# Kernel optimization log

Measured on AMD Instinct MI355X. Metric: run time of the kernel, lower is better.

The kernel has to match this reference:

```python
import jax, jax.numpy as jnp
import numpy as np

D_IN = 784
D_Z = 100
N_SAMP = 10
LOG_2PI = float(np.log(2.0 * np.pi))


def setup_inputs() -> dict:
    key = jax.random.key(0)
    ks = jax.random.split(key, 8)
    B = 16384
    x = jax.random.uniform(ks[0], (B, D_IN), dtype=jnp.float32)
    s = 0.05  # small init scale so softplus/sigmoid stay in a sane range
    W0 = jax.random.normal(ks[1], (D_Z, D_IN), dtype=jnp.float32) * s
    b0 = jax.random.normal(ks[2], (D_Z,), dtype=jnp.float32) * s
    W1 = jax.random.normal(ks[3], (D_Z, D_IN), dtype=jnp.float32) * s
    b1 = jax.random.normal(ks[4], (D_Z,), dtype=jnp.float32) * s
    W2 = jax.random.normal(ks[5], (D_IN, D_Z), dtype=jnp.float32) * s
    b2 = jax.random.normal(ks[6], (D_IN,), dtype=jnp.float32) * s
    eps = jax.random.normal(ks[7], (N_SAMP, D_Z), dtype=jnp.float32)  # pz.sample([10])
    return {"x": x, "W0": W0, "b0": b0, "W1": W1, "b1": b1, "W2": W2, "b2": b2, "eps": eps}


def reference(x, W0, b0, W1, b1, W2, b2, eps):
    # encoder: per-dim mean over the batch of softplus(Linear(x))
    mean = jnp.mean(jax.nn.softplus(x @ W0.T + b0), axis=0)        # [D_Z]
    cov = jnp.mean(jax.nn.softplus(x @ W1.T + b1), axis=0)         # [D_Z] (diag variances)
    # z = mean + covariance * eps, eps ~ N(0, I)
    z = mean + cov * eps                                           # [N_SAMP, D_Z]
    y = z @ W2.T + b2                                              # [N_SAMP, D_IN]
    p = jax.nn.sigmoid((2.0 * x[:, None, :] - 1.0) * y[None, :, :])  # [B, N_SAMP, D_IN]
    pv_z = jnp.prod(p, axis=-1) + 0.001                            # [B, N_SAMP]
    E_px_v = jnp.mean(jnp.log(pv_z))
    # diagonal-Gaussian log probs (equivalent to the MVN with eye*cov)
    log_pz = -0.5 * jnp.sum(z * z, axis=-1) - 0.5 * D_Z * LOG_2PI
    log_q = (-0.5 * jnp.sum((z - mean) ** 2 / cov, axis=-1)
             - 0.5 * jnp.sum(jnp.log(cov)) - 0.5 * D_Z * LOG_2PI)
    Dkl = jnp.mean(log_pz - log_q)
    return -(E_px_v + Dkl)
```

## Files before the change

kernel.cpp:

```cpp
#include <hip/hip_runtime.h>
#include <hip/hip_bf16.h>
#include <math.h>

#define NROWS 16384
#define DIN   784
#define DZ    100
#define NS    10
#define NCT   16
#define KTILES 25
#define BND_THR 45.0f
#define KTPAD 520

typedef unsigned short ushort_t;
typedef short bf16x8 __attribute__((ext_vector_type(8)));
typedef float f32x4  __attribute__((ext_vector_type(4)));

#define WS_Y2 208
#define WB_OFF_BYTES (64u * 1024u)

__device__ __forceinline__ float softplus_fast(float v) {
    float t = v * 1.44269504088896f;
    return (fmaxf(t, 0.f)
            + __builtin_amdgcn_logf(1.f + __builtin_amdgcn_exp2f(-fabsf(t))))
           * 0.69314718055995f;
}
__device__ __forceinline__ unsigned pack2(float lo, float hi) {
    float2 f2; f2.x = lo; f2.y = hi;
    __hip_bfloat162 h2 = __float22bfloat162_rn(f2);
    return *reinterpret_cast<unsigned*>(&h2);
}

__global__ __launch_bounds__(256) void wb_kernel(
    const float* __restrict__ W0, const float* __restrict__ W1,
    ushort_t* __restrict__ Wb, float* __restrict__ ws)
{
    if (blockIdx.x == 0) ws[threadIdx.x] = 0.f;
    int t = blockIdx.x * 256 + threadIdx.x;
    if (t >= KTILES * NCT * 64) return;
    int kt = t >> 10;
    int r  = t & 1023;
    int ct = r >> 6, l = r & 63;
    int col = ct * 16 + (l & 15);
    int k0  = kt * 32 + (l >> 4) * 8;
    uint4 o = make_uint4(0u, 0u, 0u, 0u);
    if (col < 200 && k0 < DIN) {
        const float* src = (col < 100 ? W0 + (size_t)col * DIN
                                      : W1 + (size_t)(col - 100) * DIN) + k0;
        float4 a = *(const float4*)src;
        float4 b = *(const float4*)(src + 4);
        o.x = pack2(a.x, a.y); o.y = pack2(a.z, a.w);
        o.z = pack2(b.x, b.y); o.w = pack2(b.z, b.w);
    }
    *(uint4*)(Wb + (size_t)t * 8) = o;
}

__global__ __launch_bounds__(1024) void colmean_h(
    const float* __restrict__ x, const ushort_t* __restrict__ Wb,
    const float* __restrict__ b0, const float* __restrict__ b1,
    float* __restrict__ ws)
{
    __shared__ ushort_t xls[4 * KTILES * KTPAD];
    const int tid = threadIdx.x;
    const int lane = tid & 63, w = tid >> 6;
    const int row0 = blockIdx.x * 64;

    for (int slot = tid; slot < 6400; slot += 1024) {
        int r  = slot / 100;
        int sl = slot - r * 100;
        int kt = sl >> 2, kc = sl & 3;
        int k0 = kt * 32 + kc * 8;
        uint4 o = make_uint4(0u, 0u, 0u, 0u);
        if (k0 + 8 <= DIN) {
            const float* src = x + (size_t)(row0 + r) * DIN + k0;
            float4 a = *(const float4*)src, b = *(const float4*)(src + 4);
            o.x = pack2(a.x, a.y); o.y = pack2(a.z, a.w);
            o.z = pack2(b.x, b.y); o.w = pack2(b.z, b.w);
        }
        int l = (kc << 4) | (r & 15);
        *(uint4*)&xls[((size_t)(r >> 4) * KTILES + kt) * KTPAD + l * 8] = o;
    }
    __syncthreads();

    const ushort_t* ap  = xls + lane * 8;
    const ushort_t* wbp = Wb + (size_t)w * 512 + lane * 8;

    f32x4 acc0 = (f32x4){0.f,0.f,0.f,0.f}, acc1 = acc0, acc2 = acc0, acc3 = acc0;

    bf16x8 Aa[4], Ab[4];
    uint4  Ba, Bb;

    auto ld = [&](int kt, bf16x8 (&A)[4], uint4& B) {
#pragma unroll
        for (int rt = 0; rt < 4; ++rt)
            A[rt] = *(const bf16x8*)(ap + (size_t)rt * KTILES * KTPAD + (size_t)kt * KTPAD);
        B = *(const uint4*)(wbp + (size_t)kt * 8192);
    };
    auto cp = [&](const bf16x8 (&A)[4], const uint4& B) {
        bf16x8 bf = *(const bf16x8*)&B;
        acc0 = __builtin_amdgcn_mfma_f32_16x16x32_bf16(A[0], bf, acc0, 0, 0, 0);
        acc1 = __builtin_amdgcn_mfma_f32_16x16x32_bf16(A[1], bf, acc1, 0, 0, 0);
        acc2 = __builtin_amdgcn_mfma_f32_16x16x32_bf16(A[2], bf, acc2, 0, 0, 0);
        acc3 = __builtin_amdgcn_mfma_f32_16x16x32_bf16(A[3], bf, acc3, 0, 0, 0);
    };

    ld(0, Aa, Ba);
    for (int i = 0; i < 12; ++i) {
        ld(2 * i + 1, Ab, Bb);
        cp(Aa, Ba);
        ld(2 * i + 2, Aa, Ba);
        cp(Ab, Bb);
    }
    cp(Aa, Ba);

    const int j = w * 16 + (lane & 15);
    const float bias = (j < 100) ? b0[j] : ((j < 200) ? b1[j - 100] : 0.f);
    float v = 0.f;
#pragma unroll
    for (int r = 0; r < 4; ++r)
        v += softplus_fast(acc0[r] + bias) + softplus_fast(acc1[r] + bias)
           + softplus_fast(acc2[r] + bias) + softplus_fast(acc3[r] + bias);
    v += __shfl_xor(v, 16);
    v += __shfl_xor(v, 32);
    if ((lane >> 4) == 0 && j < 200) atomicAdd(&ws[j], v);
}

__global__ __launch_bounds__(256) void y2z_kernel(
    const float* __restrict__ W2, const float* __restrict__ b2,
    const float* __restrict__ eps, float* __restrict__ ws)
{
    int wid  = (int)((blockIdx.x * 256 + threadIdx.x) >> 6);
    int lane = threadIdx.x & 63;
    if (wid >= NS * DIN) return;
    int s = wid / DIN, i = wid % DIN;
    const float inv = 1.f / (float)NROWS;
    const float* wr = W2 + (size_t)i * DZ;
    const float* er = eps + (size_t)s * DZ;
    float p = 0.f;
    for (int d = lane; d < DZ; d += 64) {
        float zd = inv * (ws[d] + ws[100 + d] * er[d]);
        p += zd * wr[d];
    }
#pragma unroll
    for (int off = 32; off > 0; off >>= 1) p += __shfl_xor(p, off);
    if (lane == 0) ws[WS_Y2 + wid] = (p + b2[i]) * 1.4426950408889634f;
}

__global__ __launch_bounds__(256, 4) void pv_final_kernel(
    const float* __restrict__ x, float* __restrict__ ws,
    const float* __restrict__ eps, float* __restrict__ out, int nblocks)
{
    __shared__ ushort_t yf[KTILES * 512];
    __shared__ ushort_t ya[KTILES * 512];
    __shared__ float bsum;
    __shared__ int lastflag;
    __shared__ float dred[256];
    const int tid = threadIdx.x;
    const int lane = tid & 63, w = tid >> 6;

    for (int idx = tid; idx < KTILES * 64; idx += 256) {
        int kt = idx >> 6, l = idx & 63;
        int ss = l & 15, k0 = kt * 32 + (l >> 4) * 8;
        uint4 o = make_uint4(0u, 0u, 0u, 0u), oa = o;
        if (ss < NS && k0 < DIN) {
            const float* src = ws + WS_Y2 + ss * DIN + k0;
            float4 a = *(const float4*)src, b = *(const float4*)(src + 4);
            o.x = pack2(a.x, a.y); o.y = pack2(a.z, a.w);
            o.z = pack2(b.x, b.y); o.w = pack2(b.z, b.w);
            oa.x = o.x & 0x7FFF7FFFu; oa.y = o.y & 0x7FFF7FFFu;
            oa.z = o.z & 0x7FFF7FFFu; oa.w = o.w & 0x7FFF7FFFu;
        }
        *(uint4*)(yf + (size_t)idx * 8) = o;
        *(uint4*)(ya + (size_t)idx * 8) = oa;
    }
    if (tid == 0) { bsum = 0.f; lastflag = 0; }
    __syncthreads();

    const int tile = blockIdx.x * 4 + w;
    const int row  = tile * 16 + (lane & 15);
    const int kc   = lane >> 4;
    const int s    = lane & 15;
    const float* xp = x + (size_t)row * DIN;
    const float L001 = -6.90775527898f;

    f32x4 acc0 = (f32x4){0.f, 0.f, 0.f, 0.f};
    f32x4 acc1 = (f32x4){0.f, 0.f, 0.f, 0.f};
    float4 a0A, a1A, a0B, a1B;

    auto loadA = [&](int kt, float4& a0, float4& a1) {
        int k0 = kt * 32 + kc * 8;
        if (k0 + 8 > DIN) k0 = 768;
        a0 = *(const float4*)(xp + k0);
        a1 = *(const float4*)(xp + k0 + 4);
    };
    auto comp = [&](int kt, const float4& a0, const float4& a1) {
        bf16x8 nf; unsigned* p = (unsigned*)&nf;
        p[0] = pack2(1.f - 2.f * a0.x, 1.f - 2.f * a0.y);
        p[1] = pack2(1.f - 2.f * a0.z, 1.f - 2.f * a0.w);
        p[2] = pack2(1.f - 2.f * a1.x, 1.f - 2.f * a1.y);
        p[3] = pack2(1.f - 2.f * a1.z, 1.f - 2.f * a1.w);
        bf16x8 na; unsigned* q = (unsigned*)&na;
        q[0] = p[0] & 0x7FFF7FFFu; q[1] = p[1] & 0x7FFF7FFFu;
        q[2] = p[2] & 0x7FFF7FFFu; q[3] = p[3] & 0x7FFF7FFFu;
        bf16x8 fy = *(const bf16x8*)(yf + (size_t)kt * 512 + lane * 8);
        bf16x8 fa = *(const bf16x8*)(ya + (size_t)kt * 512 + lane * 8);
        acc0 = __builtin_amdgcn_mfma_f32_16x16x32_bf16(nf, fy, acc0, 0, 0, 0);
        acc1 = __builtin_amdgcn_mfma_f32_16x16x32_bf16(na, fa, acc1, 0, 0, 0);
    };
    loadA(0, a0A, a1A);
    for (int i = 0; i < 12; ++i) {
        loadA(2 * i + 1, a0B, a1B);
        comp(2 * i, a0A, a1A);
        loadA(2 * i + 2, a0A, a1A);
        comp(2 * i + 1, a0B, a1B);
    }
    comp(24, a0A, a1A);

    float bnd[4];
#pragma unroll
    for (int r = 0; r < 4; ++r) bnd[r] = 0.5f * (acc0[r] + acc1[r]);
    float wsum;
    bool lslow = (s < NS) &&
        (fminf(fminf(bnd[0], bnd[1]), fminf(bnd[2], bnd[3])) < BND_THR);
    unsigned long long m = __ballot(lslow);
    if (m == 0ull) {
        wsum = 160.f * L001;
    } else {
        int nslow = 0;
        float slowsum = 0.f;
#pragma unroll
        for (int r = 0; r < 4; ++r) {
            unsigned long long mr = __ballot((s < NS) && (bnd[r] < BND_THR));
            nslow += (int)__popcll(mr);
            while (mr) {
                int src = (int)__ffsll(mr) - 1; mr &= (mr - 1);
                int ss = src & 15;
                int rrow = tile * 16 + (src >> 4) * 4 + r;
                const float* xq = x + (size_t)rrow * DIN;
                const float* yq = ws + WS_Y2 + ss * DIN;
                float a = 0.f;
                for (int i = lane; i < DIN; i += 64)
                    a -= __builtin_amdgcn_logf(
                        1.f + __builtin_amdgcn_exp2f((1.f - 2.f * xq[i]) * yq[i]));
#pragma unroll
                for (int off = 32; off > 0; off >>= 1) a += __shfl_xor(a, off);
                slowsum += __logf(__builtin_amdgcn_exp2f(a) + 0.001f);
            }
        }
        wsum = (float)(160 - nslow) * L001 + slowsum;
    }
    if (lane == 0) atomicAdd(&bsum, wsum);
    __syncthreads();

    if (tid == 0) {
        atomicAdd(&ws[200], bsum);
        __threadfence();
        unsigned old = atomicAdd((unsigned*)&ws[203], 1u);
        if (old == (unsigned)(nblocks - 1)) lastflag = 1;
    }
    __syncthreads();
    if (lastflag) {
        __threadfence();
        float contrib = 0.f;
        if (tid < DZ) {
            const float inv = 1.f / (float)NROWS;
            float mm = ws[tid] * inv;
            float cc = ws[100 + tid] * inv;
            contrib = 0.5f * __logf(cc);
#pragma unroll
            for (int ss2 = 0; ss2 < NS; ++ss2) {
                float e = eps[ss2 * DZ + tid];
                float zz = mm + cc * e;
                contrib += (0.5f * cc * e * e - 0.5f * zz * zz) * (1.f / NS);
            }
        }
        dred[tid] = contrib;
        __syncthreads();
        for (int off = 128; off > 0; off >>= 1) {
            if (tid < off) dred[tid] += dred[tid + off];
            __syncthreads();
        }
        if (tid == 0) {
            float S = atomicAdd(&ws[200], 0.f);
            float E = S * (1.f / ((float)NROWS * (float)NS));
            out[0] = -(E + dred[0]);
        }
    }
}

extern "C" void kernel_launch(void* const* d_in, const int* in_sizes, int n_in,
                              void* d_out, int out_size, void* d_ws, size_t ws_size,
                              hipStream_t stream)
{
    const float* x   = (const float*)d_in[0];
    const float* W0  = (const float*)d_in[1];
    const float* b0  = (const float*)d_in[2];
    const float* W1  = (const float*)d_in[3];
    const float* b1  = (const float*)d_in[4];
    const float* W2  = (const float*)d_in[5];
    const float* b2  = (const float*)d_in[6];
    const float* eps = (const float*)d_in[7];
    float* out = (float*)d_out;
    float* ws  = (float*)d_ws;
    ushort_t* Wb = (ushort_t*)((char*)d_ws + WB_OFF_BYTES);

    wb_kernel<<<(KTILES * NCT * 64 + 255) / 256, 256, 0, stream>>>(W0, W1, Wb, ws);
    colmean_h<<<NROWS / 64, 1024, 0, stream>>>(x, Wb, b0, b1, ws);
    y2z_kernel<<<(NS * DIN * 64) / 256, 256, 0, stream>>>(W2, b2, eps, ws);
    pv_final_kernel<<<256, 256, 0, stream>>>(x, ws, eps, out, 256);
}
```

Baseline: 50.86 us.

## Double-buffer x chunks in LDS to overlap global loads with MFMA

```diff
diff --git a/kernel.cpp b/kernel.cpp
--- a/kernel.cpp
+++ b/kernel.cpp
@@ -10,6 +10,8 @@
 #define KTILES 25
 #define BND_THR 45.0f
 #define KTPAD 520
+#define CH    5
+#define NCH   5
 
 typedef unsigned short ushort_t;
 typedef short bf16x8 __attribute__((ext_vector_type(8)));
@@ -54,63 +56,89 @@
     *(uint4*)(Wb + (size_t)t * 8) = o;
 }
 
-__global__ __launch_bounds__(1024) void colmean_h(
+__global__ __launch_bounds__(1024) void colmean_k(
     const float* __restrict__ x, const ushort_t* __restrict__ Wb,
     const float* __restrict__ b0, const float* __restrict__ b1,
     float* __restrict__ ws)
 {
-    __shared__ ushort_t xls[4 * KTILES * KTPAD];
+    __shared__ ushort_t xch[2][4 * CH * KTPAD];
     const int tid = threadIdx.x;
     const int lane = tid & 63, w = tid >> 6;
-    const int row0 = blockIdx.x * 64;
-
-    for (int slot = tid; slot < 6400; slot += 1024) {
-        int r  = slot / 100;
-        int sl = slot - r * 100;
-        int kt = sl >> 2, kc = sl & 3;
-        int k0 = kt * 32 + kc * 8;
+
+    int b = blockIdx.x;
+    int logical = (b & 7) * 32 + (b >> 3);
+    const int row0 = logical * 64;
+    const float* xr = x + (size_t)row0 * DIN;
+
+    auto stage_load = [&](int ck, int slot, uint4& s, int& doff) {
+        int r = slot / 20;
+        int rem = slot - r * 20;
+        int kt_l = rem >> 2, kc = rem & 3;
+        int k0 = (ck * CH + kt_l) * 32 + kc * 8;
         uint4 o = make_uint4(0u, 0u, 0u, 0u);
         if (k0 + 8 <= DIN) {
-            const float* src = x + (size_t)(row0 + r) * DIN + k0;
-            float4 a = *(const float4*)src, b = *(const float4*)(src + 4);
+            const float* src = xr + (size_t)r * DIN + k0;
+            float4 a = *(const float4*)src, bb = *(const float4*)(src + 4);
             o.x = pack2(a.x, a.y); o.y = pack2(a.z, a.w);
-            o.z = pack2(b.x, b.y); o.w = pack2(b.z, b.w);
-        }
+            o.z = pack2(bb.x, bb.y); o.w = pack2(bb.z, bb.w);
+        }
+        s = o;
         int l = (kc << 4) | (r & 15);
-        *(uint4*)&xls[((size_t)(r >> 4) * KTILES + kt) * KTPAD + l * 8] = o;
+        doff = ((r >> 4) * CH + kt_l) * KTPAD + l * 8;
+    };
+
+    f32x4 acc0 = (f32x4){0.f,0.f,0.f,0.f}, acc1 = acc0, acc2 = acc0, acc3 = acc0;
+    const ushort_t* wbp = Wb + (size_t)w * 512 + lane * 8;
+
+    auto compute = [&](int ck, int buf) {
+        const ushort_t* ap = xch[buf] + lane * 8;
+        uint4 Ba = *(const uint4*)(wbp + (size_t)(ck * CH) * 8192);
+#pragma unroll
+        for (int kt_l = 0; kt_l < CH; ++kt_l) {
+            uint4 Bb;
+            if (kt_l + 1 < CH)
+                Bb = *(const uint4*)(wbp + (size_t)(ck * CH + kt_l + 1) * 8192);
+            bf16x8 bf = *(const bf16x8*)&Ba;
+            bf16x8 A0 = *(const bf16x8*)(ap + (size_t)(0 * CH + kt_l) * KTPAD);
+            bf16x8 A1 = *(const bf16x8*)(ap + (size_t)(1 * CH + kt_l) * KTPAD);
+            bf16x8 A2 = *(const bf16x8*)(ap + (size_t)(2 * CH + kt_l) * KTPAD);
+            bf16x8 A3 = *(const bf16x8*)(ap + (size_t)(3 * CH + kt_l) * KTPAD);
+            acc0 = __builtin_amdgcn_mfma_f32_16x16x32_bf16(A0, bf, acc0, 0, 0, 0);
+            acc1 = __builtin_amdgcn_mfma_f32_16x16x32_bf16(A1, bf, acc1, 0, 0, 0);
+            acc2 = __builtin_amdgcn_mfma_f32_16x16x32_bf16(A2, bf, acc2, 0, 0, 0);
+            acc3 = __builtin_amdgcn_mfma_f32_16x16x32_bf16(A3, bf, acc3, 0, 0, 0);
+            Ba = Bb;
+        }
+    };
+
+    {
+        uint4 s0, s1; int d0, d1;
+        stage_load(0, tid, s0, d0);
+        bool two = (tid < 1280 - 1024);
+        if (two) stage_load(0, tid + 1024, s1, d1);
+        *(uint4*)&xch[0][d0] = s0;
+        if (two) *(uint4*)&xch[0][d1] = s1;
     }
     __syncthreads();
 
-    const ushort_t* ap  = xls + lane * 8;
-    const ushort_t* wbp = Wb + (size_t)w * 512 + lane * 8;
-
-    f32x4 acc0 = (f32x4){0.f,0.f,0.f,0.f}, acc1 = acc0, acc2 = acc0, acc3 = acc0;
-
-    bf16x8 Aa[4], Ab[4];
-    uint4  Ba, Bb;
-
-    auto ld = [&](int kt, bf16x8 (&A)[4], uint4& B) {
-#pragma unroll
-        for (int rt = 0; rt < 4; ++rt)
-            A[rt] = *(const bf16x8*)(ap + (size_t)rt * KTILES * KTPAD + (size_t)kt * KTPAD);
-        B = *(const uint4*)(wbp + (size_t)kt * 8192);
-    };
-    auto cp = [&](const bf16x8 (&A)[4], const uint4& B) {
-        bf16x8 bf = *(const bf16x8*)&B;
-        acc0 = __builtin_amdgcn_mfma_f32_16x16x32_bf16(A[0], bf, acc0, 0, 0, 0);
-        acc1 = __builtin_amdgcn_mfma_f32_16x16x32_bf16(A[1], bf, acc1, 0, 0, 0);
-        acc2 = __builtin_amdgcn_mfma_f32_16x16x32_bf16(A[2], bf, acc2, 0, 0, 0);
-        acc3 = __builtin_amdgcn_mfma_f32_16x16x32_bf16(A[3], bf, acc3, 0, 0, 0);
-    };
-
-    ld(0, Aa, Ba);
-    for (int i = 0; i < 12; ++i) {
-        ld(2 * i + 1, Ab, Bb);
-        cp(Aa, Ba);
-        ld(2 * i + 2, Aa, Ba);
-        cp(Ab, Bb);
-    }
-    cp(Aa, Ba);
+    int cur = 0;
+#pragma unroll 1
+    for (int ck = 0; ck < NCH; ++ck) {
+        uint4 s0, s1; int d0, d1;
+        const bool more = (ck + 1 < NCH);
+        const bool two = (tid < 1280 - 1024);
+        if (more) {
+            stage_load(ck + 1, tid, s0, d0);
+            if (two) stage_load(ck + 1, tid + 1024, s1, d1);
+        }
+        compute(ck, cur);
+        if (more) {
+            *(uint4*)&xch[cur ^ 1][d0] = s0;
+            if (two) *(uint4*)&xch[cur ^ 1][d1] = s1;
+        }
+        __syncthreads();
+        cur ^= 1;
+    }
 
     const int j = w * 16 + (lane & 15);
     const float bias = (j < 100) ? b0[j] : ((j < 200) ? b1[j - 100] : 0.f);
@@ -304,7 +332,7 @@
     ushort_t* Wb = (ushort_t*)((char*)d_ws + WB_OFF_BYTES);
 
     wb_kernel<<<(KTILES * NCT * 64 + 255) / 256, 256, 0, stream>>>(W0, W1, Wb, ws);
-    colmean_h<<<NROWS / 64, 1024, 0, stream>>>(x, Wb, b0, b1, ws);
+    colmean_k<<<256, 1024, 0, stream>>>(x, Wb, b0, b1, ws);
     y2z_kernel<<<(NS * DIN * 64) / 256, 256, 0, stream>>>(W2, b2, eps, ws);
     pv_final_kernel<<<256, 256, 0, stream>>>(x, ws, eps, out, 256);
 }
```

Result: slower. 53.97 us (+6.1%).

## Switch encoder GEMM to 32x32x16 MFMA tiles with repacked weights and LDS layout

Applied to the files above, without the earlier changes.

```diff
diff --git a/kernel.cpp b/kernel.cpp
--- a/kernel.cpp
+++ b/kernel.cpp
@@ -6,14 +6,16 @@
 #define DIN   784
 #define DZ    100
 #define NS    10
-#define NCT   16
 #define KTILES 25
+#define KT32  49
+#define NCT32 7
 #define BND_THR 45.0f
-#define KTPAD 520
+#define KTP2  520
 
 typedef unsigned short ushort_t;
 typedef short bf16x8 __attribute__((ext_vector_type(8)));
 typedef float f32x4  __attribute__((ext_vector_type(4)));
+typedef float f32x16 __attribute__((ext_vector_type(16)));
 
 #define WS_Y2 208
 #define WB_OFF_BYTES (64u * 1024u)
@@ -30,20 +32,20 @@
     return *reinterpret_cast<unsigned*>(&h2);
 }
 
-__global__ __launch_bounds__(256) void wb_kernel(
+__global__ __launch_bounds__(256) void wb2_kernel(
     const float* __restrict__ W0, const float* __restrict__ W1,
     ushort_t* __restrict__ Wb, float* __restrict__ ws)
 {
     if (blockIdx.x == 0) ws[threadIdx.x] = 0.f;
     int t = blockIdx.x * 256 + threadIdx.x;
-    if (t >= KTILES * NCT * 64) return;
-    int kt = t >> 10;
-    int r  = t & 1023;
-    int ct = r >> 6, l = r & 63;
-    int col = ct * 16 + (l & 15);
-    int k0  = kt * 32 + (l >> 4) * 8;
+    if (t >= KT32 * NCT32 * 64) return;
+    int kt  = t / (NCT32 * 64);
+    int rem = t - kt * (NCT32 * 64);
+    int ct = rem >> 6, l = rem & 63;
+    int col = ct * 32 + (l & 31);
+    int k0  = kt * 16 + (l >> 5) * 8;
     uint4 o = make_uint4(0u, 0u, 0u, 0u);
-    if (col < 200 && k0 < DIN) {
+    if (col < 200) {
         const float* src = (col < 100 ? W0 + (size_t)col * DIN
                                       : W1 + (size_t)(col - 100) * DIN) + k0;
         float4 a = *(const float4*)src;
@@ -54,57 +56,52 @@
     *(uint4*)(Wb + (size_t)t * 8) = o;
 }
 
-__global__ __launch_bounds__(1024) void colmean_h(
+__global__ __launch_bounds__(896) void colmean_m(
     const float* __restrict__ x, const ushort_t* __restrict__ Wb,
     const float* __restrict__ b0, const float* __restrict__ b1,
     float* __restrict__ ws)
 {
-    __shared__ ushort_t xls[4 * KTILES * KTPAD];
+    __shared__ ushort_t xls[2 * KT32 * KTP2];
     const int tid = threadIdx.x;
     const int lane = tid & 63, w = tid >> 6;
     const int row0 = blockIdx.x * 64;
 
-    for (int slot = tid; slot < 6400; slot += 1024) {
-        int r  = slot / 100;
-        int sl = slot - r * 100;
-        int kt = sl >> 2, kc = sl & 3;
-        int k0 = kt * 32 + kc * 8;
-        uint4 o = make_uint4(0u, 0u, 0u, 0u);
-        if (k0 + 8 <= DIN) {
-            const float* src = x + (size_t)(row0 + r) * DIN + k0;
-            float4 a = *(const float4*)src, b = *(const float4*)(src + 4);
-            o.x = pack2(a.x, a.y); o.y = pack2(a.z, a.w);
-            o.z = pack2(b.x, b.y); o.w = pack2(b.z, b.w);
-        }
-        int l = (kc << 4) | (r & 15);
-        *(uint4*)&xls[((size_t)(r >> 4) * KTILES + kt) * KTPAD + l * 8] = o;
+#pragma unroll
+    for (int i = 0; i < 7; ++i) {
+        int slot = tid + i * 896;
+        int r  = slot / 98;
+        int sc = slot - r * 98;
+        int kt = sc >> 1, kg = sc & 1;
+        const float* src = x + (size_t)(row0 + r) * DIN + sc * 8;
+        float4 a = *(const float4*)src, b = *(const float4*)(src + 4);
+        uint4 o;
+        o.x = pack2(a.x, a.y); o.y = pack2(a.z, a.w);
+        o.z = pack2(b.x, b.y); o.w = pack2(b.z, b.w);
+        int l = kg * 32 + (r & 31);
+        *(uint4*)&xls[((size_t)(r >> 5) * KT32 + kt) * KTP2 + l * 8] = o;
     }
     __syncthreads();
 
-    const ushort_t* ap  = xls + lane * 8;
-    const ushort_t* wbp = Wb + (size_t)w * 512 + lane * 8;
-
-    f32x4 acc0 = (f32x4){0.f,0.f,0.f,0.f}, acc1 = acc0, acc2 = acc0, acc3 = acc0;
-
-    bf16x8 Aa[4], Ab[4];
+    const int rt = w & 1, ct = w >> 1;
+    const ushort_t* ap  = xls + (size_t)rt * KT32 * KTP2 + lane * 8;
+    const ushort_t* wbp = Wb + (size_t)ct * 512 + lane * 8;
+
+    f32x16 acc;
+#pragma unroll
+    for (int r = 0; r < 16; ++r) acc[r] = 0.f;
+
+    bf16x8 Aa, Ab;
     uint4  Ba, Bb;
-
-    auto ld = [&](int kt, bf16x8 (&A)[4], uint4& B) {
-#pragma unroll
-        for (int rt = 0; rt < 4; ++rt)
-            A[rt] = *(const bf16x8*)(ap + (size_t)rt * KTILES * KTPAD + (size_t)kt * KTPAD);
-        B = *(const uint4*)(wbp + (size_t)kt * 8192);
+    auto ld = [&](int kt, bf16x8& A, uint4& B) {
+        A = *(const bf16x8*)(ap + (size_t)kt * KTP2);
+        B = *(const uint4*)(wbp + (size_t)kt * (NCT32 * 512));
     };
-    auto cp = [&](const bf16x8 (&A)[4], const uint4& B) {
-        bf16x8 bf = *(const bf16x8*)&B;
-        acc0 = __builtin_amdgcn_mfma_f32_16x16x32_bf16(A[0], bf, acc0, 0, 0, 0);
-        acc1 = __builtin_amdgcn_mfma_f32_16x16x32_bf16(A[1], bf, acc1, 0, 0, 0);
-        acc2 = __builtin_amdgcn_mfma_f32_16x16x32_bf16(A[2], bf, acc2, 0, 0, 0);
-        acc3 = __builtin_amdgcn_mfma_f32_16x16x32_bf16(A[3], bf, acc3, 0, 0, 0);
+    auto cp = [&](const bf16x8& A, const uint4& B) {
+        acc = __builtin_amdgcn_mfma_f32_32x32x16_bf16(A, *(const bf16x8*)&B, acc, 0, 0, 0);
     };
 
     ld(0, Aa, Ba);
-    for (int i = 0; i < 12; ++i) {
+    for (int i = 0; i < 24; ++i) {
         ld(2 * i + 1, Ab, Bb);
         cp(Aa, Ba);
         ld(2 * i + 2, Aa, Ba);
@@ -112,16 +109,13 @@
     }
     cp(Aa, Ba);
 
-    const int j = w * 16 + (lane & 15);
+    const int j = ct * 32 + (lane & 31);
     const float bias = (j < 100) ? b0[j] : ((j < 200) ? b1[j - 100] : 0.f);
     float v = 0.f;
 #pragma unroll
-    for (int r = 0; r < 4; ++r)
-        v += softplus_fast(acc0[r] + bias) + softplus_fast(acc1[r] + bias)
-           + softplus_fast(acc2[r] + bias) + softplus_fast(acc3[r] + bias);
-    v += __shfl_xor(v, 16);
+    for (int r = 0; r < 16; ++r) v += softplus_fast(acc[r] + bias);
     v += __shfl_xor(v, 32);
-    if ((lane >> 4) == 0 && j < 200) atomicAdd(&ws[j], v);
+    if (lane < 32 && j < 200) atomicAdd(&ws[j], v);
 }
 
 __global__ __launch_bounds__(256) void y2z_kernel(
@@ -303,8 +297,8 @@
     float* ws  = (float*)d_ws;
     ushort_t* Wb = (ushort_t*)((char*)d_ws + WB_OFF_BYTES);
 
-    wb_kernel<<<(KTILES * NCT * 64 + 255) / 256, 256, 0, stream>>>(W0, W1, Wb, ws);
-    colmean_h<<<NROWS / 64, 1024, 0, stream>>>(x, Wb, b0, b1, ws);
+    wb2_kernel<<<(KT32 * NCT32 * 64 + 255) / 256, 256, 0, stream>>>(W0, W1, Wb, ws);
+    colmean_m<<<NROWS / 64, 896, 0, stream>>>(x, Wb, b0, b1, ws);
     y2z_kernel<<<(NS * DIN * 64) / 256, 256, 0, stream>>>(W2, b2, eps, ws);
     pv_final_kernel<<<256, 256, 0, stream>>>(x, ws, eps, out, 256);
 }
```

New measurement: 57.12 us. +12.3%, slower.
